# Kernel optimization log

Measured on AMD Instinct MI355X. Metric: run time of the kernel, lower is better.

## Reference

```python
import jax, jax.numpy as jnp
import numpy as np

H, W = 96, 96
SIGMA_PX = 1.5
ZMIN, ZMAX = 0.2, 10.0
FX = FY = 60.0


def setup_inputs() -> dict:
    key = jax.random.key(0)
    k1, k2 = jax.random.split(key)
    B, K, N = 4, 8, 256
    # x,y spread so projections land around the image; z inside z_clip
    xy = jax.random.normal(k1, (B, K, N, 2), dtype=jnp.float32) * 1.5
    z = jax.random.uniform(k2, (B, K, N, 1), dtype=jnp.float32, minval=0.5, maxval=5.0)
    points_world = jnp.concatenate([xy, z], axis=-1)  # (B,K,N,3)
    return {"points_world": points_world}


def reference(points_world):
    # points_world: (B,K,N,3) -> image (B,1,H,W)
    dt = points_world.dtype
    cx = (W - 1) / 2.0
    cy = (H - 1) / 2.0
    x = points_world[..., 0]
    y = points_world[..., 1]
    z = jnp.maximum(points_world[..., 2], 0.001)
    valid = ((z > ZMIN) & (z < ZMAX)).astype(dt)  # (B,K,N)
    u = FX * (x / z) + cx  # (B,K,N)
    v = FY * (y / z) + cy
    gx = jnp.arange(W, dtype=dt)  # pixel x coords
    gy = jnp.arange(H, dtype=dt)  # pixel y coords
    # Isotropic Gaussian is separable: exp(-0.5*(dx^2+dy^2)) = ex * ey
    ex = jnp.exp(-0.5 * ((gx[None, None, None, :] - u[..., None]) / SIGMA_PX) ** 2)  # (B,K,N,W)
    ey = jnp.exp(-0.5 * ((gy[None, None, None, :] - v[..., None]) / SIGMA_PX) ** 2)  # (B,K,N,H)
    ey = ey * valid[..., None]
    # sum over K and N point splats -> (B,H,W)
    img = jnp.einsum('bknh,bknw->bhw', ey, ex)
    img = 1.0 - jnp.exp(-img)
    return img[:, None, :, :]  # (B,1,H,W)
```

## Files before the change

kernel.cpp:

```cpp
#include <hip/hip_runtime.h>
#include <hip/hip_fp16.h>


#define HDIM 96
#define WDIM 96
#define PIX   (HDIM * WDIM)
#define HHALF 48
#define PTS_PER_BATCH 2048
#define P_CHUNK 64
#define CHUNKS  32
#define BATCHES 4
#define NPART   (BATCHES * CHUNKS)

__global__ __launch_bounds__(256)
void splat_partial_kernel(const float* __restrict__ pts, __half* __restrict__ ws) {
    __shared__ float sex[P_CHUNK][WDIM];
    __shared__ float sey[P_CHUNK][HHALF];
    __shared__ float su[P_CHUNK], sv[P_CHUNK];

    const int b    = blockIdx.x >> 6;
    const int c    = (blockIdx.x >> 1) & (CHUNKS - 1);
    const int half = blockIdx.x & 1;
    const int t = threadIdx.x;

    if (t < P_CHUNK) {
        const int p = (b * PTS_PER_BATCH + c * P_CHUNK + t) * 3;
        const float x = pts[p + 0];
        const float y = pts[p + 1];
        float z = fmaxf(pts[p + 2], 0.001f);
        const bool valid = (z > 0.2f && z < 10.0f);
        const float inv = __frcp_rn(z);
        su[t] = 60.0f * x * inv + 47.5f;
        sv[t] = valid ? (60.0f * y * inv + 47.5f) : 1.0e9f;
    }
    __syncthreads();

    const float kcoef = -1.0f / (2.0f * 1.5f * 1.5f);
    const float rowbase = (float)(half * HHALF);
    for (int i = t; i < P_CHUNK * WDIM; i += 256) {
        const int p = i / WDIM;
        const int cidx = i - p * WDIM;
        const float du = (float)cidx - su[p];
        sex[p][cidx] = __expf(kcoef * du * du);
    }
    for (int i = t; i < P_CHUNK * HHALF; i += 256) {
        const int p = i / HHALF;
        const int r = i - p * HHALF;
        const float dv = rowbase + (float)r - sv[p];
        sey[p][r] = __expf(kcoef * dv * dv);
    }
    __syncthreads();

    const int tw = t & 15;
    const int th = t >> 4;
    const int w0 = tw * 6;
    const int r0 = th * 3;

    float acc[3][6];
#pragma unroll
    for (int i = 0; i < 3; ++i)
#pragma unroll
        for (int j = 0; j < 6; ++j) acc[i][j] = 0.0f;

#pragma unroll
    for (int p = 0; p < P_CHUNK; ++p) {
        const float2 e0 = *(const float2*)&sex[p][w0 + 0];
        const float2 e1 = *(const float2*)&sex[p][w0 + 2];
        const float2 e2 = *(const float2*)&sex[p][w0 + 4];
        const float ex[6] = { e0.x, e0.y, e1.x, e1.y, e2.x, e2.y };
        float ey[3];
#pragma unroll
        for (int i = 0; i < 3; ++i) ey[i] = sey[p][r0 + i];
#pragma unroll
        for (int i = 0; i < 3; ++i)
#pragma unroll
            for (int j = 0; j < 6; ++j) acc[i][j] = fmaf(ey[i], ex[j], acc[i][j]);
    }

    const int part = b * CHUNKS + c;
    __half* base = ws + (size_t)part * PIX;
#pragma unroll
    for (int i = 0; i < 3; ++i) {
        __half2* dst = (__half2*)&base[(half * HHALF + r0 + i) * WDIM + w0];
#pragma unroll
        for (int q = 0; q < 3; ++q)
            dst[q] = __floats2half2_rn(acc[i][2*q + 0], acc[i][2*q + 1]);
    }
}

__global__ __launch_bounds__(256)
void reduce_finish_kernel(const __half2* __restrict__ ws, float2* __restrict__ out) {
    const int g = blockIdx.x * 256 + threadIdx.x;
    const int b = g / (PIX / 2);
    const int i = g - b * (PIX / 2);

    const __half2* src = ws + (size_t)b * CHUNKS * (PIX / 2) + i;

    float2 s0 = make_float2(0.f, 0.f), s1 = s0, s2 = s0, s3 = s0;
#pragma unroll
    for (int c = 0; c < CHUNKS; c += 4) {
        const float2 v0 = __half22float2(src[(size_t)(c + 0) * (PIX / 2)]);
        const float2 v1 = __half22float2(src[(size_t)(c + 1) * (PIX / 2)]);
        const float2 v2 = __half22float2(src[(size_t)(c + 2) * (PIX / 2)]);
        const float2 v3 = __half22float2(src[(size_t)(c + 3) * (PIX / 2)]);
        s0.x += v0.x; s0.y += v0.y;
        s1.x += v1.x; s1.y += v1.y;
        s2.x += v2.x; s2.y += v2.y;
        s3.x += v3.x; s3.y += v3.y;
    }
    const float sx = (s0.x + s1.x) + (s2.x + s3.x);
    const float sy = (s0.y + s1.y) + (s2.y + s3.y);

    out[g] = make_float2(1.0f - __expf(-sx), 1.0f - __expf(-sy));
}

extern "C" void kernel_launch(void* const* d_in, const int* in_sizes, int n_in,
                              void* d_out, int out_size, void* d_ws, size_t ws_size,
                              hipStream_t stream) {
    const float* pts = (const float*)d_in[0];
    __half* ws = (__half*)d_ws;
    float2* out = (float2*)d_out;

    splat_partial_kernel<<<NPART * 2, 256, 0, stream>>>(pts, ws);
    reduce_finish_kernel<<<(BATCHES * PIX / 2) / 256, 256, 0, stream>>>(
        (const __half2*)ws, out);
}
```

Before: 61.28 us.

## Fuse splat and reduce via cooperative grid sync, skip far-away points per wavefront

Merges the partial-splat and reduce/finish kernels into one cooperative kernel separated by a grid-wide barrier, removing a second launch and the gap between kernels. Each wavefront also skips points whose projected row lies more than about 10 pixels outside its 12-row band, which avoids FMAs on contributions that are negligible. The cost is the grid.sync overhead and a requirement that all 256 blocks be co-resident. The culling also drops tails of exp(-22) or smaller, so the output is approximate.

```diff
diff --git a/kernel.cpp b/kernel.cpp
--- a/kernel.cpp
+++ b/kernel.cpp
@@ -1,5 +1,8 @@
 #include <hip/hip_runtime.h>
 #include <hip/hip_fp16.h>
+#include <hip/hip_cooperative_groups.h>
+
+namespace cg = cooperative_groups;
 
 
 #define HDIM 96
@@ -11,9 +14,13 @@
 #define CHUNKS  32
 #define BATCHES 4
 #define NPART   (BATCHES * CHUNKS)
+#define NBLOCKS (NPART * 2)
+#define NH2     (BATCHES * PIX / 2)
 
 __global__ __launch_bounds__(256)
-void splat_partial_kernel(const float* __restrict__ pts, __half* __restrict__ ws) {
+void fused_render_kernel(const float* __restrict__ pts,
+                         __half* __restrict__ ws,
+                         float2* __restrict__ out) {
     __shared__ float sex[P_CHUNK][WDIM];
     __shared__ float sey[P_CHUNK][HHALF];
     __shared__ float su[P_CHUNK], sv[P_CHUNK];
@@ -56,14 +63,19 @@
     const int w0 = tw * 6;
     const int r0 = th * 3;
 
+    const float wlo = rowbase + (float)(12 * (t >> 6)) - 10.0f;
+    const float whi = wlo + 31.0f;
+
     float acc[3][6];
 #pragma unroll
     for (int i = 0; i < 3; ++i)
 #pragma unroll
         for (int j = 0; j < 6; ++j) acc[i][j] = 0.0f;
 
-#pragma unroll
+#pragma unroll 4
     for (int p = 0; p < P_CHUNK; ++p) {
+        const float vp = sv[p];
+        if (vp < wlo || vp > whi) continue;
         const float2 e0 = *(const float2*)&sex[p][w0 + 0];
         const float2 e1 = *(const float2*)&sex[p][w0 + 2];
         const float2 e2 = *(const float2*)&sex[p][w0 + 4];
@@ -77,41 +89,42 @@
             for (int j = 0; j < 6; ++j) acc[i][j] = fmaf(ey[i], ex[j], acc[i][j]);
     }
 
-    const int part = b * CHUNKS + c;
-    __half* base = ws + (size_t)part * PIX;
+    {
+        const int part = b * CHUNKS + c;
+        __half* base = ws + (size_t)part * PIX;
 #pragma unroll
-    for (int i = 0; i < 3; ++i) {
-        __half2* dst = (__half2*)&base[(half * HHALF + r0 + i) * WDIM + w0];
+        for (int i = 0; i < 3; ++i) {
+            __half2* dst = (__half2*)&base[(half * HHALF + r0 + i) * WDIM + w0];
 #pragma unroll
-        for (int q = 0; q < 3; ++q)
-            dst[q] = __floats2half2_rn(acc[i][2*q + 0], acc[i][2*q + 1]);
+            for (int q = 0; q < 3; ++q)
+                dst[q] = __floats2half2_rn(acc[i][2*q + 0], acc[i][2*q + 1]);
+        }
     }
-}
 
-__global__ __launch_bounds__(256)
-void reduce_finish_kernel(const __half2* __restrict__ ws, float2* __restrict__ out) {
-    const int g = blockIdx.x * 256 + threadIdx.x;
-    const int b = g / (PIX / 2);
-    const int i = g - b * (PIX / 2);
+    cg::this_grid().sync();
 
-    const __half2* src = ws + (size_t)b * CHUNKS * (PIX / 2) + i;
+    const int g = blockIdx.x * 256 + t;
+    if (g < NH2) {
+        const int bb = g / (PIX / 2);
+        const int i = g - bb * (PIX / 2);
+        const __half2* src = (const __half2*)ws + (size_t)bb * CHUNKS * (PIX / 2) + i;
 
-    float2 s0 = make_float2(0.f, 0.f), s1 = s0, s2 = s0, s3 = s0;
+        float2 s0 = make_float2(0.f, 0.f), s1 = s0, s2 = s0, s3 = s0;
 #pragma unroll
-    for (int c = 0; c < CHUNKS; c += 4) {
-        const float2 v0 = __half22float2(src[(size_t)(c + 0) * (PIX / 2)]);
-        const float2 v1 = __half22float2(src[(size_t)(c + 1) * (PIX / 2)]);
-        const float2 v2 = __half22float2(src[(size_t)(c + 2) * (PIX / 2)]);
-        const float2 v3 = __half22float2(src[(size_t)(c + 3) * (PIX / 2)]);
-        s0.x += v0.x; s0.y += v0.y;
-        s1.x += v1.x; s1.y += v1.y;
-        s2.x += v2.x; s2.y += v2.y;
-        s3.x += v3.x; s3.y += v3.y;
+        for (int cc = 0; cc < CHUNKS; cc += 4) {
+            const float2 v0 = __half22float2(src[(size_t)(cc + 0) * (PIX / 2)]);
+            const float2 v1 = __half22float2(src[(size_t)(cc + 1) * (PIX / 2)]);
+            const float2 v2 = __half22float2(src[(size_t)(cc + 2) * (PIX / 2)]);
+            const float2 v3 = __half22float2(src[(size_t)(cc + 3) * (PIX / 2)]);
+            s0.x += v0.x; s0.y += v0.y;
+            s1.x += v1.x; s1.y += v1.y;
+            s2.x += v2.x; s2.y += v2.y;
+            s3.x += v3.x; s3.y += v3.y;
+        }
+        const float sx = (s0.x + s1.x) + (s2.x + s3.x);
+        const float sy = (s0.y + s1.y) + (s2.y + s3.y);
+        out[g] = make_float2(1.0f - __expf(-sx), 1.0f - __expf(-sy));
     }
-    const float sx = (s0.x + s1.x) + (s2.x + s3.x);
-    const float sy = (s0.y + s1.y) + (s2.y + s3.y);
-
-    out[g] = make_float2(1.0f - __expf(-sx), 1.0f - __expf(-sy));
 }
 
 extern "C" void kernel_launch(void* const* d_in, const int* in_sizes, int n_in,
@@ -121,7 +134,7 @@
     __half* ws = (__half*)d_ws;
     float2* out = (float2*)d_out;
 
-    splat_partial_kernel<<<NPART * 2, 256, 0, stream>>>(pts, ws);
-    reduce_finish_kernel<<<(BATCHES * PIX / 2) / 256, 256, 0, stream>>>(
-        (const __half2*)ws, out);
+    void* args[] = { (void*)&pts, (void*)&ws, (void*)&out };
+    hipLaunchCooperativeKernel((const void*)fused_render_kernel,
+                               dim3(NBLOCKS), dim3(256), args, 0, stream);
 }
```

Result: slower. 98.15 us (+60.1%).
